# Optimization experiments

Measured on AMD Instinct MI355X. Metric: run time of the kernel, lower is better.

## Reference

```python
import jax, jax.numpy as jnp
import numpy as np

B, S, DIM = 2, 512, 4096
SMAX = 4096
HQ, HKV, HD = 32, 8, 128
REP = HQ // HKV
THETA = 1e6
NEG = -1e9  # stands in for -inf in the causal mask (safe under softmax/vjp)


def setup_inputs() -> dict:
    key = jax.random.key(0)
    ks = jax.random.split(key, 8)
    x = jax.random.normal(ks[0], (B, S, DIM), jnp.float32)
    # RoPE tables (complex freqs_cis represented as cos/sin), rope_theta=1e6
    inv = 1.0 / (THETA ** (np.arange(0, HD, 2, dtype=np.float64) / HD))
    ang = np.arange(SMAX, dtype=np.float64)[:, None] * inv[None, :]
    freqs_cos = jnp.asarray(np.cos(ang), jnp.float32)  # [SMAX, HD//2]
    freqs_sin = jnp.asarray(np.sin(ang), jnp.float32)
    cache = jax.random.normal(ks[1], (2, 1, B, SMAX, HKV, HD), jnp.float32) * 0.02
    i = np.arange(SMAX)
    mask = jnp.asarray(np.where(i[None, :] <= i[:, None], 0.0, NEG), jnp.float32)
    storage_idx = jnp.arange(S, dtype=jnp.int32)
    sc = 0.02
    wq = jax.random.normal(ks[2], (HQ * HD, DIM), jnp.float32) * sc
    wk = jax.random.normal(ks[3], (HKV * HD, DIM), jnp.float32) * sc
    wv = jax.random.normal(ks[4], (HKV * HD, DIM), jnp.float32) * sc
    wo = jax.random.normal(ks[5], (DIM, HQ * HD), jnp.float32) * sc
    return {"x": x, "freqs_cos": freqs_cos, "freqs_sin": freqs_sin, "cache": cache,
            "mask": mask, "storage_idx": storage_idx, "wq": wq, "wk": wk, "wv": wv, "wo": wo}


def _rope(t, c, s):
    # t: [B,S,H,HD]; consecutive pairs (2i, 2i+1) form complex numbers
    tr = t.reshape(*t.shape[:-1], -1, 2)
    a, b = tr[..., 0], tr[..., 1]
    o0 = a * c - b * s
    o1 = a * s + b * c
    return jnp.stack([o0, o1], axis=-1).reshape(t.shape)


def reference(x, freqs_cos, freqs_sin, cache, mask, storage_idx, wq, wk, wv, wo):
    bsz, seqlen, _ = x.shape
    hd = cache.shape[-1]
    hkv = cache.shape[-2]
    hq = wq.shape[0] // hd
    rep = hq // hkv
    xq = (x @ wq.T).reshape(bsz, seqlen, hq, hd)
    xk = (x @ wk.T).reshape(bsz, seqlen, hkv, hd)
    xv = (x @ wv.T).reshape(bsz, seqlen, hkv, hd)
    c = freqs_cos[storage_idx][None, :, None, :]  # [1,S,1,HD//2]
    s = freqs_sin[storage_idx][None, :, None, :]
    xq = _rope(xq, c, s)
    xk = _rope(xk, c, s)
    # rotating-cache write (index_copy along seq dim of cache[0/1, li])
    k_cache = cache[0, 0].at[:, storage_idx].set(xk)  # [B,SMAX,HKV,HD]
    v_cache = cache[1, 0].at[:, storage_idx].set(xv)
    keys = jnp.repeat(k_cache, rep, axis=2)    # GQA expand -> [B,SMAX,HQ,HD]
    values = jnp.repeat(v_cache, rep, axis=2)
    # NOTE: faithful to source: scores = QK^T / (head_dim ** -0.5)
    scores = jnp.einsum('bqhd,bkhd->bhqk', xq, keys) / (hd ** -0.5)
    scores = scores + mask[storage_idx][None, None, :, :]
    probs = jax.nn.softmax(scores.astype(jnp.float32), axis=-1).astype(xq.dtype)
    out = jnp.einsum('bhqk,bkhd->bqhd', probs, values).reshape(bsz, seqlen, hq * hd)
    return out @ wo.T
```

## Files before the change

kernel.cpp:

```cpp
#include <hip/hip_runtime.h>

#define Bn   2
#define Sn   512
#define DIMn 4096
#define HQn  32
#define HKVn 8
#define HDn  128
#define NPAIR 64
#define KVN  (HKVn * HDn)
#define NALL (DIMn + 2 * KVN)
#define SCALE 11.313708498984761f

typedef short bf16x8 __attribute__((ext_vector_type(8)));
typedef float f32x4 __attribute__((ext_vector_type(4)));
typedef unsigned short ushort8 __attribute__((ext_vector_type(8)));
typedef unsigned short ushort4s __attribute__((ext_vector_type(4)));
typedef int i32x4 __attribute__((ext_vector_type(4)));

__device__ __forceinline__ unsigned short f2bf_rne(float f) {
  unsigned u = __builtin_bit_cast(unsigned, f);
  u += 0x7fffu + ((u >> 16) & 1u);
  return (unsigned short)(u >> 16);
}
__device__ __forceinline__ float bf2f(unsigned short h) {
  unsigned u = ((unsigned)h) << 16;
  return __builtin_bit_cast(float, u);
}
__device__ __forceinline__ void split_bf16(float x, unsigned short& hi, unsigned short& lo) {
  unsigned u = __builtin_bit_cast(unsigned, x);
  hi = (unsigned short)(u >> 16);
  float hf = __builtin_bit_cast(float, u & 0xffff0000u);
  lo = (unsigned short)(__builtin_bit_cast(unsigned, x - hf) >> 16);
}
__device__ __forceinline__ void gload16(const void* g, void* lds) {
  __builtin_amdgcn_global_load_lds(
      (const __attribute__((address_space(1))) unsigned int*)g,
      (__attribute__((address_space(3))) unsigned int*)lds, 16, 0, 0);
}

__global__ __launch_bounds__(256) void quant_rows(
    const float* __restrict__ x, const float* __restrict__ wq,
    const float* __restrict__ wk, const float* __restrict__ wv,
    const float* __restrict__ wo,
    signed char* __restrict__ xh8, signed char* __restrict__ xl8,
    signed char* __restrict__ wh8, signed char* __restrict__ wl8,
    unsigned short* __restrict__ woh,
    float* __restrict__ sA, float* __restrict__ sW)
{
  const int r = blockIdx.x;
  const int t = threadIdx.x;

  if (r >= 1024 + NALL) {
    int wr2 = r - 1024 - NALL;
    const float* src = wo + (size_t)wr2 * DIMn;
    unsigned short* dst = woh + (size_t)wr2 * DIMn;
    #pragma unroll
    for (int j = 0; j < 4; ++j) {
      float4 v = ((const float4*)src)[t + j * 256];
      ushort4s h;
      h[0] = f2bf_rne(v.x); h[1] = f2bf_rne(v.y);
      h[2] = f2bf_rne(v.z); h[3] = f2bf_rne(v.w);
      ((ushort4s*)dst)[t + j * 256] = h;
    }
    return;
  }

  const float* src; signed char* ph; signed char* pl; float* ps; size_t prow;
  if (r < 1024) {
    src = x + (size_t)r * DIMn; ph = xh8; pl = xl8; ps = sA + r; prow = (size_t)r * DIMn;
  } else {
    int wr_ = r - 1024;
    ps = sW + wr_; ph = wh8; pl = wl8; prow = (size_t)wr_ * DIMn;
    if (wr_ < DIMn)            src = wq + (size_t)wr_ * DIMn;
    else if (wr_ < DIMn + KVN) src = wk + (size_t)(wr_ - DIMn) * DIMn;
    else                       src = wv + (size_t)(wr_ - DIMn - KVN) * DIMn;
  }
  float4 v[4];
  float am = 0.f;
  #pragma unroll
  for (int j = 0; j < 4; ++j) {
    v[j] = ((const float4*)src)[t + j * 256];
    am = fmaxf(am, fmaxf(fmaxf(fabsf(v[j].x), fabsf(v[j].y)),
                         fmaxf(fabsf(v[j].z), fabsf(v[j].w))));
  }
  #pragma unroll
  for (int o = 1; o < 64; o <<= 1) am = fmaxf(am, __shfl_xor(am, o));
  __shared__ float wm[4];
  if ((t & 63) == 0) wm[t >> 6] = am;
  __syncthreads();
  am = fmaxf(fmaxf(wm[0], wm[1]), fmaxf(wm[2], wm[3]));
  const float inv = (am > 0.f) ? 32512.0f / am : 0.f;
  if (t == 0) *ps = am * (1.0f / 32512.0f);
  #pragma unroll
  for (int j = 0; j < 4; ++j) {
    float fv[4] = {v[j].x, v[j].y, v[j].z, v[j].w};
    signed char hh[4], ll[4];
    #pragma unroll
    for (int e = 0; e < 4; ++e) {
      int q = __float2int_rn(fv[e] * inv);
      int hi = (q + 128) >> 8;
      hh[e] = (signed char)hi;
      ll[e] = (signed char)(q - (hi << 8));
    }
    ((char4*)(ph + prow))[t + j * 256] = make_char4(hh[0], hh[1], hh[2], hh[3]);
    ((char4*)(pl + prow))[t + j * 256] = make_char4(ll[0], ll[1], ll[2], ll[3]);
  }
}

__global__ __launch_bounds__(256, 2) void qkv_gemm_i8(
    const signed char* __restrict__ Ah, const signed char* __restrict__ Al,
    const signed char* __restrict__ Wh, const signed char* __restrict__ Wl,
    const float* __restrict__ sA, const float* __restrict__ sW,
    float* __restrict__ CQ, float* __restrict__ CK, unsigned short* __restrict__ CV)
{
  constexpr int KS = 64;
  constexpr int TILEB = 224 * 128;
  __shared__ __align__(16) signed char Ls[2][TILEB];

  const int t = threadIdx.x, w = t >> 6, lane = t & 63;
  const int bid = blockIdx.x;
  const int s = (bid & 7) * 64 + (bid >> 3);
  const int bx = s >> 3, by = s & 7;
  const int bm = by * 128, bn = bx * 96;

  const signed char* gsrc[7];
  int ldst[7];
  #pragma unroll
  for (int j = 0; j < 4; ++j) {
    int u = j * 256 + t;
    int R = u >> 3, slot = u & 7;
    int q = slot ^ (R & 7);
    gsrc[j] = (q < 4 ? Ah : Al) + (size_t)(bm + R) * DIMn + (q & 3) * 16;
    ldst[j] = u * 16;
  }
  #pragma unroll
  for (int j = 4; j < 7; ++j) {
    int base0 = (j - 4) * 16;
    int rb = base0 + (t >> 3) + ((t < 128) ? 0 : 32);
    int slot = t & 7;
    int q = slot ^ (rb & 7);
    gsrc[j] = (q < 4 ? Wh : Wl) + (size_t)(bn + rb) * DIMn + (q & 3) * 16;
    ldst[j] = (128 + rb) * 128 + slot * 16;
  }

  const int wr = w >> 1, wc = w & 1;
  const int rl = lane & 15, kh = lane >> 4;
  int aoff[4], boff[3];
  #pragma unroll
  for (int fm = 0; fm < 4; ++fm) {
    int R = wr * 64 + fm * 16 + rl;
    aoff[fm] = R * 128 + ((kh ^ (R & 7)) * 16);
  }
  #pragma unroll
  for (int fn = 0; fn < 3; ++fn) {
    int R = 128 + wc * 48 + fn * 16 + rl;
    boff[fn] = R * 128 + ((kh ^ (R & 7)) * 16);
  }

  i32x4 acc1[4][3], acc2[4][3];
  #pragma unroll
  for (int i = 0; i < 4; ++i)
  #pragma unroll
    for (int j = 0; j < 3; ++j) {
      acc1[i][j] = (i32x4){0, 0, 0, 0};
      acc2[i][j] = (i32x4){0, 0, 0, 0};
    }

  const int nt = DIMn / KS;
  #pragma unroll
  for (int j = 0; j < 7; ++j) gload16(gsrc[j], &Ls[0][ldst[j]]);

  for (int tt = 0; tt < nt; ++tt) {
    const int buf = tt & 1, nbuf = buf ^ 1;
    const bool more = (tt + 1 < nt);
    const signed char* Lp = &Ls[buf][0];
    i32x4 ah[4], al[4];

    asm volatile("s_waitcnt vmcnt(2)" ::: "memory");
    __builtin_amdgcn_s_barrier();
    __builtin_amdgcn_sched_barrier(0);
    if (more) {
      #pragma unroll
      for (int j = 0; j < 5; ++j)
        gload16(gsrc[j] + (size_t)(tt + 1) * KS, &Ls[nbuf][ldst[j]]);
    }
    #pragma unroll
    for (int fm = 0; fm < 4; ++fm) {
      ah[fm] = *(const i32x4*)(Lp + aoff[fm]);
      al[fm] = *(const i32x4*)(Lp + (aoff[fm] ^ 64));
    }
    {
      i32x4 bh = *(const i32x4*)(Lp + boff[0]);
      i32x4 bl = *(const i32x4*)(Lp + (boff[0] ^ 64));
      __builtin_amdgcn_s_setprio(1);
      #pragma unroll
      for (int fm = 0; fm < 4; ++fm) {
        acc1[fm][0] = __builtin_amdgcn_mfma_i32_16x16x64_i8(ah[fm], bh, acc1[fm][0], 0, 0, 0);
        acc2[fm][0] = __builtin_amdgcn_mfma_i32_16x16x64_i8(ah[fm], bl, acc2[fm][0], 0, 0, 0);
        acc2[fm][0] = __builtin_amdgcn_mfma_i32_16x16x64_i8(al[fm], bh, acc2[fm][0], 0, 0, 0);
      }
      __builtin_amdgcn_s_setprio(0);
    }

    if (more) asm volatile("s_waitcnt vmcnt(6)" ::: "memory");
    else      asm volatile("s_waitcnt vmcnt(1)" ::: "memory");
    __builtin_amdgcn_s_barrier();
    __builtin_amdgcn_sched_barrier(0);
    if (more)
      gload16(gsrc[5] + (size_t)(tt + 1) * KS, &Ls[nbuf][ldst[5]]);
    {
      i32x4 bh = *(const i32x4*)(Lp + boff[1]);
      i32x4 bl = *(const i32x4*)(Lp + (boff[1] ^ 64));
      __builtin_amdgcn_s_setprio(1);
      #pragma unroll
      for (int fm = 0; fm < 4; ++fm) {
        acc1[fm][1] = __builtin_amdgcn_mfma_i32_16x16x64_i8(ah[fm], bh, acc1[fm][1], 0, 0, 0);
        acc2[fm][1] = __builtin_amdgcn_mfma_i32_16x16x64_i8(ah[fm], bl, acc2[fm][1], 0, 0, 0);
        acc2[fm][1] = __builtin_amdgcn_mfma_i32_16x16x64_i8(al[fm], bh, acc2[fm][1], 0, 0, 0);
      }
      __builtin_amdgcn_s_setprio(0);
    }

    if (more) asm volatile("s_waitcnt vmcnt(6)" ::: "memory");
    else      asm volatile("s_waitcnt vmcnt(0)" ::: "memory");
    __builtin_amdgcn_s_barrier();
    __builtin_amdgcn_sched_barrier(0);
    if (more)
      gload16(gsrc[6] + (size_t)(tt + 1) * KS, &Ls[nbuf][ldst[6]]);
    {
      i32x4 bh = *(const i32x4*)(Lp + boff[2]);
      i32x4 bl = *(const i32x4*)(Lp + (boff[2] ^ 64));
      __builtin_amdgcn_s_setprio(1);
      #pragma unroll
      for (int fm = 0; fm < 4; ++fm) {
        acc1[fm][2] = __builtin_amdgcn_mfma_i32_16x16x64_i8(ah[fm], bh, acc1[fm][2], 0, 0, 0);
        acc2[fm][2] = __builtin_amdgcn_mfma_i32_16x16x64_i8(ah[fm], bl, acc2[fm][2], 0, 0, 0);
        acc2[fm][2] = __builtin_amdgcn_mfma_i32_16x16x64_i8(al[fm], bh, acc2[fm][2], 0, 0, 0);
      }
      __builtin_amdgcn_s_setprio(0);
    }
  }

  #pragma unroll
  for (int fn = 0; fn < 3; ++fn) {
    const int colW = bn + wc * 48 + fn * 16 + rl;
    const float sw = sW[colW];
    #pragma unroll
    for (int fm = 0; fm < 4; ++fm) {
      #pragma unroll
      for (int j = 0; j < 4; ++j) {
        int grow = bm + wr * 64 + fm * 16 + kh * 4 + j;
        float val = sA[grow] * sw *
            fmaf((float)acc1[fm][fn][j], 65536.0f, (float)acc2[fm][fn][j] * 256.0f);
        if (colW < DIMn)            CQ[(size_t)grow * DIMn + colW] = val;
        else if (colW < DIMn + KVN) CK[(size_t)grow * KVN + (colW - DIMn)] = val;
        else                        CV[(size_t)grow * KVN + (colW - DIMn - KVN)] = f2bf_rne(val);
      }
    }
  }
}

template<bool SPLIT, int OMODE>
__global__ __launch_bounds__(256, 2) void pgemm3(
    const unsigned short* __restrict__ Ah, const unsigned short* __restrict__ Al,
    const unsigned short* __restrict__ Wh, const unsigned short* __restrict__ Wl,
    void* __restrict__ C0, void* __restrict__ C1, void* __restrict__ C2, int Kd)
{
  constexpr int BM = 128, BN = 64;
  constexpr int ROWS = BM + BN;
  constexpr int UPT = ROWS / 32;
  constexpr int KS = SPLIT ? 32 : 64;
  constexpr int TILEB = ROWS * 128;

  __shared__ __align__(16) unsigned char Ls[3 * TILEB];

  const int t = threadIdx.x, w = t >> 6, lane = t & 63;
  const int bid = blockIdx.x;
  const int s = (bid & 7) * 64 + (bid >> 3);
  const int bm = (s & 7) * BM, bn = (s >> 3) * BN;

  const unsigned short* gsrc[UPT];
  #pragma unroll
  for (int j = 0; j < UPT; ++j) {
    int u = j * 256 + t;
    int R = u >> 3;
    int q = (u & 7) ^ (R & 7);
    int chunk = SPLIT ? (q & 3) : q;
    bool lo_ = SPLIT && (q >= 4);
    const unsigned short* base = (R < BM) ? (lo_ ? Al : Ah) : (lo_ ? Wl : Wh);
    int rg = (R < BM) ? (bm + R) : (bn + (R - BM));
    gsrc[j] = base + (size_t)rg * Kd + chunk * 8;
  }

  const int wr = w >> 1, wc = w & 1;
  const int rl = lane & 15, kh = lane >> 4;
  int aoff[4], boff[2];
  #pragma unroll
  for (int fm = 0; fm < 4; ++fm) {
    int r = wr * 64 + fm * 16 + rl;
    aoff[fm] = r * 128 + ((kh ^ (r & 7)) * 16);
  }
  #pragma unroll
  for (int fn = 0; fn < 2; ++fn) {
    int r = BM + wc * 32 + fn * 16 + rl;
    boff[fn] = r * 128 + ((kh ^ (r & 7)) * 16);
  }

  f32x4 acc[4][2];
  #pragma unroll
  for (int i = 0; i < 4; ++i)
  #pragma unroll
    for (int j = 0; j < 2; ++j) acc[i][j] = (f32x4){0.f, 0.f, 0.f, 0.f};

  const int nt = Kd / KS;
  #pragma unroll
  for (int j = 0; j < UPT; ++j) gload16(gsrc[j], &Ls[0 * TILEB + (j * 256 + t) * 16]);
  #pragma unroll
  for (int j = 0; j < UPT; ++j) gload16(gsrc[j] + KS, &Ls[1 * TILEB + (j * 256 + t) * 16]);

  int cur = 0;
  for (int tt = 0; tt < nt; ++tt) {
    if (tt + 1 < nt) asm volatile("s_waitcnt vmcnt(%0)" :: "n"(UPT) : "memory");
    else             asm volatile("s_waitcnt vmcnt(0)" ::: "memory");
    __builtin_amdgcn_s_barrier();
    __builtin_amdgcn_sched_barrier(0);

    int pre = cur + 2; if (pre >= 3) pre -= 3;
    if (tt + 2 < nt) {
      #pragma unroll
      for (int j = 0; j < UPT; ++j)
        gload16(gsrc[j] + (size_t)(tt + 2) * KS, &Ls[pre * TILEB + (j * 256 + t) * 16]);
    }

    const unsigned char* Lp = &Ls[cur * TILEB];
    bf16x8 a0[4], a1[4], b0[2], b1[2];
    #pragma unroll
    for (int fm = 0; fm < 4; ++fm) {
      a0[fm] = *(const bf16x8*)(Lp + aoff[fm]);
      a1[fm] = *(const bf16x8*)(Lp + (aoff[fm] ^ 64));
    }
    #pragma unroll
    for (int fn = 0; fn < 2; ++fn) {
      b0[fn] = *(const bf16x8*)(Lp + boff[fn]);
      b1[fn] = *(const bf16x8*)(Lp + (boff[fn] ^ 64));
    }
    __builtin_amdgcn_s_setprio(1);
    #pragma unroll
    for (int fm = 0; fm < 4; ++fm)
    #pragma unroll
      for (int fn = 0; fn < 2; ++fn) {
        if constexpr (SPLIT) {
          acc[fm][fn] = __builtin_amdgcn_mfma_f32_16x16x32_bf16(a0[fm], b0[fn], acc[fm][fn], 0, 0, 0);
          acc[fm][fn] = __builtin_amdgcn_mfma_f32_16x16x32_bf16(a1[fm], b0[fn], acc[fm][fn], 0, 0, 0);
          acc[fm][fn] = __builtin_amdgcn_mfma_f32_16x16x32_bf16(a0[fm], b1[fn], acc[fm][fn], 0, 0, 0);
        } else {
          acc[fm][fn] = __builtin_amdgcn_mfma_f32_16x16x32_bf16(a0[fm], b0[fn], acc[fm][fn], 0, 0, 0);
          acc[fm][fn] = __builtin_amdgcn_mfma_f32_16x16x32_bf16(a1[fm], b1[fn], acc[fm][fn], 0, 0, 0);
        }
      }
    __builtin_amdgcn_s_setprio(0);
    cur += 1; if (cur >= 3) cur -= 3;
  }

  const int crow0 = bm + wr * 64 + kh * 4;
  #pragma unroll
  for (int fm = 0; fm < 4; ++fm)
  #pragma unroll
    for (int fn = 0; fn < 2; ++fn)
    #pragma unroll
      for (int j = 0; j < 4; ++j) {
        int row = crow0 + fm * 16 + j;
        float v = acc[fm][fn][j];
        int col = bn + wc * 32 + fn * 16 + rl;
        if constexpr (OMODE == 0) {
          ((float*)C0)[(size_t)row * DIMn + col] = v;
        } else {
          if (col < DIMn)
            ((float*)C0)[(size_t)row * DIMn + col] = v;
          else if (col < DIMn + KVN)
            ((float*)C1)[(size_t)row * KVN + (col - DIMn)] = v;
          else
            ((unsigned short*)C2)[(size_t)row * KVN + (col - DIMn - KVN)] = f2bf_rne(v);
        }
      }
}

template<bool SPLIT, int BN>
__global__ __launch_bounds__(256, 2) void gemm_mfma(
    const float* __restrict__ A,
    const float* __restrict__ W0, float* __restrict__ C0,
    const float* __restrict__ W1, float* __restrict__ C1,
    int Kd, int N)
{
  constexpr int BM = 64;
  constexpr int KSTEP = SPLIT ? 32 : 64;
  constexpr int CPR = SPLIT ? 4 : 8;
  constexpr int AUNITS = BM * KSTEP / 8;
  constexpr int UNITS  = (BM + BN) * KSTEP / 8;
  constexpr int UPT = UNITS / 256;
  constexpr int FN = BN / 32;
  constexpr int ROWS = BM + BN;

  __shared__ __align__(16) unsigned short Ls[2][ROWS * 64];

  const float* __restrict__ W = (blockIdx.z == 0) ? W0 : W1;
  float* __restrict__ Cp = (blockIdx.z == 0) ? C0 : C1;

  const int t  = threadIdx.x;
  const int bm = blockIdx.y * BM;
  const int bn = blockIdx.x * BN;

  const float* gsrc[UPT];
  int loff[UPT];
  #pragma unroll
  for (int i = 0; i < UPT; ++i) {
    int u = i * 256 + t;
    int row, c;
    if (u < AUNITS) {
      row = u / CPR; c = u % CPR;
      gsrc[i] = A + (size_t)(bm + row) * Kd + c * 8;
    } else {
      int v = u - AUNITS;
      int rr = v / CPR; c = v % CPR;
      row = BM + rr;
      gsrc[i] = W + (size_t)(bn + rr) * Kd + c * 8;
    }
    loff[i] = row * 64 + (c ^ (row & 7)) * 8;
  }

  const int lane = t & 63;
  const int w  = t >> 6;
  const int wr = w >> 1, wc = w & 1;
  const int rl = lane & 15, kh = lane >> 4;

  int aoff[2], boff[FN];
  #pragma unroll
  for (int fm = 0; fm < 2; ++fm) {
    int row = wr * 32 + fm * 16 + rl;
    aoff[fm] = row * 64 + (kh ^ (row & 7)) * 8;
  }
  #pragma unroll
  for (int fn = 0; fn < FN; ++fn) {
    int row = BM + wc * (BN / 2) + fn * 16 + rl;
    boff[fn] = row * 64 + (kh ^ (row & 7)) * 8;
  }

  f32x4 acc[2][FN];
  #pragma unroll
  for (int i = 0; i < 2; ++i)
  #pragma unroll
    for (int j = 0; j < FN; ++j) acc[i][j] = (f32x4){0.f, 0.f, 0.f, 0.f};

  float4 f0[UPT], f1[UPT];
  #pragma unroll
  for (int i = 0; i < UPT; ++i) {
    f0[i] = *(const float4*)(gsrc[i]);
    f1[i] = *(const float4*)(gsrc[i] + 4);
  }

  const int nt = Kd / KSTEP;
  for (int tt = 0; tt < nt; ++tt) {
    unsigned short* Lp = &Ls[tt & 1][0];
    #pragma unroll
    for (int i = 0; i < UPT; ++i) {
      float xv[8] = {f0[i].x, f0[i].y, f0[i].z, f0[i].w,
                     f1[i].x, f1[i].y, f1[i].z, f1[i].w};
      ushort8 hi, lo;
      #pragma unroll
      for (int j = 0; j < 8; ++j) {
        if constexpr (SPLIT) {
          unsigned short h_, l_;
          split_bf16(xv[j], h_, l_);
          hi[j] = h_; lo[j] = l_;
        } else {
          hi[j] = f2bf_rne(xv[j]);
          lo[j] = 0;
        }
      }
      *(ushort8*)(Lp + loff[i]) = hi;
      if constexpr (SPLIT)
        *(ushort8*)(((uintptr_t)(Lp + loff[i])) ^ 64) = lo;
    }
    if (tt + 1 < nt) {
      #pragma unroll
      for (int i = 0; i < UPT; ++i) {
        f0[i] = *(const float4*)(gsrc[i] + (size_t)(tt + 1) * KSTEP);
        f1[i] = *(const float4*)(gsrc[i] + (size_t)(tt + 1) * KSTEP + 4);
      }
    }
    __syncthreads();

    bf16x8 a0[2], a1[2], b0[FN], b1[FN];
    #pragma unroll
    for (int fm = 0; fm < 2; ++fm) {
      const unsigned short* p = Lp + aoff[fm];
      a0[fm] = *(const bf16x8*)p;
      a1[fm] = *(const bf16x8*)(((uintptr_t)p) ^ 64);
    }
    #pragma unroll
    for (int fn = 0; fn < FN; ++fn) {
      const unsigned short* p = Lp + boff[fn];
      b0[fn] = *(const bf16x8*)p;
      b1[fn] = *(const bf16x8*)(((uintptr_t)p) ^ 64);
    }
    #pragma unroll
    for (int fm = 0; fm < 2; ++fm)
    #pragma unroll
      for (int fn = 0; fn < FN; ++fn) {
        if constexpr (SPLIT) {
          acc[fm][fn] = __builtin_amdgcn_mfma_f32_16x16x32_bf16(a0[fm], b0[fn], acc[fm][fn], 0, 0, 0);
          acc[fm][fn] = __builtin_amdgcn_mfma_f32_16x16x32_bf16(a1[fm], b0[fn], acc[fm][fn], 0, 0, 0);
          acc[fm][fn] = __builtin_amdgcn_mfma_f32_16x16x32_bf16(a0[fm], b1[fn], acc[fm][fn], 0, 0, 0);
        } else {
          acc[fm][fn] = __builtin_amdgcn_mfma_f32_16x16x32_bf16(a0[fm], b0[fn], acc[fm][fn], 0, 0, 0);
          acc[fm][fn] = __builtin_amdgcn_mfma_f32_16x16x32_bf16(a1[fm], b1[fn], acc[fm][fn], 0, 0, 0);
        }
      }
  }

  const int crow0 = bm + wr * 32 + kh * 4;
  const int ccol0 = bn + wc * (BN / 2) + rl;
  #pragma unroll
  for (int fm = 0; fm < 2; ++fm)
  #pragma unroll
    for (int fn = 0; fn < FN; ++fn)
    #pragma unroll
      for (int j = 0; j < 4; ++j)
        Cp[(size_t)(crow0 + fm * 16 + j) * N + ccol0 + fn * 16] = acc[fm][fn][j];
}

#define KT 32

template<bool BF16IO>
__global__ __launch_bounds__(256, 2) void flash_attn_mfma(
    const float* __restrict__ Qg, const float* __restrict__ Kg, const void* __restrict__ Vgv,
    const float* __restrict__ fc, const float* __restrict__ fs,
    const int* __restrict__ sidx, void* __restrict__ Ov)
{
  const int bid = blockIdx.x;
  const int qt = bid & 7;
  const int h  = (bid >> 3) & 31;
  const int b  = bid >> 8;
  const int q0 = qt * 64;
  const int hk = h >> 2;

  __shared__ __align__(16) unsigned short Ks[2][2][32][128];
  __shared__ __align__(16) unsigned short Vt[2][128][40];

  const int t = threadIdx.x;
  const int w = t >> 6;
  const int lane = t & 63;
  const int rl = lane & 15;
  const int kh = lane >> 4;

  const int qrow = q0 + w * 16 + rl;
  const int qp = sidx[qrow];

  int kr[2], kc_[2];
  #pragma unroll
  for (int i = 0; i < 2; ++i) { int u = i * 256 + t; kr[i] = u >> 4; kc_[i] = u & 15; }
  const int kkv = t >> 3, dcv = t & 7;

  const int nkt = (q0 + 64) / KT;
  const int qmaxw = q0 + w * 16 + 15;

  float kreg[2][8]; float4 kc4[2], ks4[2];
  float vregf[16];
  ushort8 vregu[2];

  #pragma unroll
  for (int i = 0; i < 2; ++i) {
    const float* kp_ = Kg + ((size_t)(b * Sn + kr[i]) * HKVn + hk) * HDn + kc_[i] * 8;
    *(float4*)&kreg[i][0] = *(const float4*)kp_;
    *(float4*)&kreg[i][4] = *(const float4*)(kp_ + 4);
    int posk = sidx[kr[i]];
    kc4[i] = *(const float4*)(fc + (size_t)posk * NPAIR + kc_[i] * 4);
    ks4[i] = *(const float4*)(fs + (size_t)posk * NPAIR + kc_[i] * 4);
  }
  if constexpr (BF16IO) {
    const unsigned short* vp_ = (const unsigned short*)Vgv +
        ((size_t)(b * Sn + kkv) * HKVn + hk) * HDn + dcv * 16;
    vregu[0] = *(const ushort8*)vp_;
    vregu[1] = *(const ushort8*)(vp_ + 8);
  } else {
    const float* vp_ = (const float*)Vgv + ((size_t)(b * Sn + kkv) * HKVn + hk) * HDn + dcv * 16;
    #pragma unroll
    for (int i = 0; i < 4; ++i) *(float4*)&vregf[i * 4] = *(const float4*)(vp_ + i * 4);
  }

  bf16x8 qh[4], ql[4];
  {
    const float* qptr = Qg + ((size_t)(b * Sn + qrow) * HQn + h) * HDn;
    #pragma unroll
    for (int ds = 0; ds < 4; ++ds) {
      int d0 = ds * 32 + kh * 8;
      float4 u0 = *(const float4*)(qptr + d0);
      float4 u1 = *(const float4*)(qptr + d0 + 4);
      float4 c4 = *(const float4*)(fc + (size_t)qp * NPAIR + d0 / 2);
      float4 s4 = *(const float4*)(fs + (size_t)qp * NPAIR + d0 / 2);
      float v[8];
      v[0] = u0.x * c4.x - u0.y * s4.x;  v[1] = u0.x * s4.x + u0.y * c4.x;
      v[2] = u0.z * c4.y - u0.w * s4.y;  v[3] = u0.z * s4.y + u0.w * c4.y;
      v[4] = u1.x * c4.z - u1.y * s4.z;  v[5] = u1.x * s4.z + u1.y * c4.z;
      v[6] = u1.z * c4.w - u1.w * s4.w;  v[7] = u1.z * s4.w + u1.w * c4.w;
      #pragma unroll
      for (int j = 0; j < 8; ++j) {
        unsigned short h_, l_;
        split_bf16(v[j], h_, l_);
        qh[ds][j] = (short)h_; ql[ds][j] = (short)l_;
      }
    }
  }

  float m_run = -3.0e38f, l_run = 0.f;
  f32x4 acc_o[8];
  #pragma unroll
  for (int i = 0; i < 8; ++i) acc_o[i] = (f32x4){0.f, 0.f, 0.f, 0.f};

  for (int tt = 0; tt < nkt; ++tt) {
    const int kbase = tt * KT;
    const int buf = tt & 1;

    #pragma unroll
    for (int i = 0; i < 2; ++i) {
      float rv[8];
      rv[0] = kreg[i][0] * kc4[i].x - kreg[i][1] * ks4[i].x;
      rv[1] = kreg[i][0] * ks4[i].x + kreg[i][1] * kc4[i].x;
      rv[2] = kreg[i][2] * kc4[i].y - kreg[i][3] * ks4[i].y;
      rv[3] = kreg[i][2] * ks4[i].y + kreg[i][3] * kc4[i].y;
      rv[4] = kreg[i][4] * kc4[i].z - kreg[i][5] * ks4[i].z;
      rv[5] = kreg[i][4] * ks4[i].z + kreg[i][5] * kc4[i].z;
      rv[6] = kreg[i][6] * kc4[i].w - kreg[i][7] * ks4[i].w;
      rv[7] = kreg[i][6] * ks4[i].w + kreg[i][7] * kc4[i].w;
      ushort8 hi, lo;
      #pragma unroll
      for (int j = 0; j < 8; ++j) {
        unsigned short h_, l_;
        split_bf16(rv[j], h_, l_);
        hi[j] = h_; lo[j] = l_;
      }
      int slot = kc_[i] ^ (kr[i] & 15);
      *(ushort8*)&Ks[buf][0][kr[i]][slot * 8] = hi;
      *(ushort8*)&Ks[buf][1][kr[i]][slot * 8] = lo;
    }
    if constexpr (BF16IO) {
      #pragma unroll
      for (int i = 0; i < 8; ++i) {
        Vt[buf][dcv * 16 + i][kkv] = vregu[0][i];
        Vt[buf][dcv * 16 + 8 + i][kkv] = vregu[1][i];
      }
    } else {
      #pragma unroll
      for (int i = 0; i < 16; ++i)
        Vt[buf][dcv * 16 + i][kkv] = f2bf_rne(vregf[i]);
    }

    if (tt + 1 < nkt) {
      const int kb = kbase + KT;
      #pragma unroll
      for (int i = 0; i < 2; ++i) {
        const float* kp_ = Kg + ((size_t)(b * Sn + kb + kr[i]) * HKVn + hk) * HDn + kc_[i] * 8;
        *(float4*)&kreg[i][0] = *(const float4*)kp_;
        *(float4*)&kreg[i][4] = *(const float4*)(kp_ + 4);
        int posk = sidx[kb + kr[i]];
        kc4[i] = *(const float4*)(fc + (size_t)posk * NPAIR + kc_[i] * 4);
        ks4[i] = *(const float4*)(fs + (size_t)posk * NPAIR + kc_[i] * 4);
      }
      if constexpr (BF16IO) {
        const unsigned short* vp_ = (const unsigned short*)Vgv +
            ((size_t)(b * Sn + kb + kkv) * HKVn + hk) * HDn + dcv * 16;
        vregu[0] = *(const ushort8*)vp_;
        vregu[1] = *(const ushort8*)(vp_ + 8);
      } else {
        const float* vp_ = (const float*)Vgv + ((size_t)(b * Sn + kb + kkv) * HKVn + hk) * HDn + dcv * 16;
        #pragma unroll
        for (int i = 0; i < 4; ++i) *(float4*)&vregf[i * 4] = *(const float4*)(vp_ + i * 4);
      }
    }
    __syncthreads();

    if (kbase > qmaxw) continue;

    float p[8];
    #pragma unroll
    for (int fm = 0; fm < 2; ++fm) {
      f32x4 accs = (f32x4){0.f, 0.f, 0.f, 0.f};
      #pragma unroll
      for (int ds = 0; ds < 4; ++ds) {
        int slot = (ds * 4 + kh) ^ rl;
        bf16x8 kH = *(const bf16x8*)&Ks[buf][0][fm * 16 + rl][slot * 8];
        bf16x8 kL = *(const bf16x8*)&Ks[buf][1][fm * 16 + rl][slot * 8];
        accs = __builtin_amdgcn_mfma_f32_16x16x32_bf16(kH, qh[ds], accs, 0, 0, 0);
        accs = __builtin_amdgcn_mfma_f32_16x16x32_bf16(kL, qh[ds], accs, 0, 0, 0);
        accs = __builtin_amdgcn_mfma_f32_16x16x32_bf16(kH, ql[ds], accs, 0, 0, 0);
      }
      #pragma unroll
      for (int r = 0; r < 4; ++r) {
        int kp = kbase + fm * 16 + kh * 4 + r;
        p[fm * 4 + r] = accs[r] * SCALE + ((kp <= qp) ? 0.f : -1.0e9f);
      }
    }

    float tmax = p[0];
    #pragma unroll
    for (int i = 1; i < 8; ++i) tmax = fmaxf(tmax, p[i]);
    tmax = fmaxf(tmax, __shfl_xor(tmax, 16));
    tmax = fmaxf(tmax, __shfl_xor(tmax, 32));
    float m_new = fmaxf(m_run, tmax);
    float crs = __expf(m_run - m_new);
    m_run = m_new;
    float tsum = 0.f;
    bf16x8 pa;
    #pragma unroll
    for (int i = 0; i < 8; ++i) {
      float ev = __expf(p[i] - m_new);
      tsum += ev;
      pa[i] = (short)f2bf_rne(ev);
    }
    tsum += __shfl_xor(tsum, 16);
    tsum += __shfl_xor(tsum, 32);
    l_run = l_run * crs + tsum;

    float cq[4];
    #pragma unroll
    for (int r = 0; r < 4; ++r) cq[r] = __shfl(crs, kh * 4 + r);

    #pragma unroll
    for (int db = 0; db < 8; ++db) {
      short4 v0 = *(const short4*)&Vt[buf][db * 16 + rl][kh * 4];
      short4 v1 = *(const short4*)&Vt[buf][db * 16 + rl][16 + kh * 4];
      bf16x8 vb = {v0.x, v0.y, v0.z, v0.w, v1.x, v1.y, v1.z, v1.w};
      f32x4 a = acc_o[db];
      a[0] *= cq[0]; a[1] *= cq[1]; a[2] *= cq[2]; a[3] *= cq[3];
      acc_o[db] = __builtin_amdgcn_mfma_f32_16x16x32_bf16(pa, vb, a, 0, 0, 0);
    }
  }

  float lq[4];
  #pragma unroll
  for (int r = 0; r < 4; ++r) lq[r] = 1.0f / __shfl(l_run, kh * 4 + r);
  #pragma unroll
  for (int db = 0; db < 8; ++db)
  #pragma unroll
    for (int r = 0; r < 4; ++r) {
      int q = q0 + w * 16 + kh * 4 + r;
      size_t idx = ((size_t)(b * Sn + q) * HQn + h) * HDn + db * 16 + rl;
      float val = acc_o[db][r] * lq[r];
      if constexpr (BF16IO) ((unsigned short*)Ov)[idx] = f2bf_rne(val);
      else                  ((float*)Ov)[idx] = val;
    }
}

extern "C" void kernel_launch(void* const* d_in, const int* in_sizes, int n_in,
                              void* d_out, int out_size, void* d_ws, size_t ws_size,
                              hipStream_t stream)
{
  const float* x    = (const float*)d_in[0];
  const float* fc   = (const float*)d_in[1];
  const float* fs   = (const float*)d_in[2];
  const int*   sidx = (const int*)d_in[5];
  const float* wq   = (const float*)d_in[6];
  const float* wk   = (const float*)d_in[7];
  const float* wv   = (const float*)d_in[8];
  const float* wo   = (const float*)d_in[9];
  float* out = (float*)d_out;

  const int M = Bn * Sn;
  const size_t EX  = (size_t)M * DIMn;
  const size_t EW  = (size_t)DIMn * DIMn;
  const size_t EK  = (size_t)M * KVN;
  const size_t EX8 = EX;
  const size_t EW8 = (size_t)NALL * DIMn;

  char* p = (char*)d_ws;
  signed char* xh8 = (signed char*)p;        p += EX8;
  signed char* xl8 = (signed char*)p;        p += EX8;
  signed char* wh8 = (signed char*)p;        p += EW8;
  signed char* wl8 = (signed char*)p;        p += EW8;
  float* sA = (float*)p;                     p += 1024 * 4;
  float* sW = (float*)p;                     p += (size_t)NALL * 4;
  float* Qw = (float*)p;                     p += 4 * EX;
  float* Kw = (float*)p;                     p += 4 * EK;
  unsigned short* Vw = (unsigned short*)p;   p += 2 * EK;
  unsigned short* woh = (unsigned short*)p;  p += 2 * EW;
  unsigned short* Aw = (unsigned short*)p;   p += 2 * EX;
  const size_t NEED = (size_t)(p - (char*)d_ws);

  if (ws_size >= NEED) {
    quant_rows<<<1024 + NALL + DIMn, 256, 0, stream>>>(
        x, wq, wk, wv, wo, xh8, xl8, wh8, wl8, woh, sA, sW);
    qkv_gemm_i8<<<512, 256, 0, stream>>>(
        xh8, xl8, wh8, wl8, sA, sW, Qw, Kw, Vw);
    flash_attn_mfma<true><<<Bn * HQn * (Sn / 64), 256, 0, stream>>>(
        Qw, Kw, Vw, fc, fs, sidx, Aw);
    pgemm3<false, 0><<<512, 256, 0, stream>>>(
        Aw, Aw, woh, woh, out, nullptr, nullptr, DIMn);
  } else {
    float* Qw2 = (float*)d_ws;
    float* Kw2 = Qw2 + (size_t)M * HQn * HDn;
    float* Vw2 = Kw2 + (size_t)M * HKVn * HDn;
    float* Aw2 = Vw2 + (size_t)M * HKVn * HDn;
    gemm_mfma<true, 128><<<dim3(DIMn / 128, M / 64, 1), 256, 0, stream>>>(
        x, wq, Qw2, wq, Qw2, DIMn, DIMn);
    gemm_mfma<true, 64><<<dim3((HKVn * HDn) / 64, M / 64, 2), 256, 0, stream>>>(
        x, wk, Kw2, wv, Vw2, DIMn, HKVn * HDn);
    flash_attn_mfma<false><<<Bn * HQn * (Sn / 64), 256, 0, stream>>>(
        Qw2, Kw2, Vw2, fc, fs, sidx, Aw2);
    gemm_mfma<false, 128><<<dim3(DIMn / 128, M / 64, 1), 256, 0, stream>>>(
        Aw2, wo, out, wo, out, DIMn, DIMn);
  }
}
```

Before: 215.9 us.

## Quantize output projection to int8 with per-row weight and global activation scales

Replaces the bf16 output-projection GEMM with an int8 MFMA GEMM. Wo is quantized per row to int8 inside the prep kernel. The attention kernel now tracks a global abs-max of its output through an atomic, and a new kernel quantizes the bf16 attention output to int8 with that single scale. This halves operand bytes and uses the faster int8 MFMA rate, at the cost of an extra quantization pass, an atomic reduction, and coarser numerical precision from per-tensor activation scaling.

```diff
diff --git a/kernel.cpp b/kernel.cpp
--- a/kernel.cpp
+++ b/kernel.cpp
@@ -14,7 +14,7 @@
 typedef short bf16x8 __attribute__((ext_vector_type(8)));
 typedef float f32x4 __attribute__((ext_vector_type(4)));
 typedef unsigned short ushort8 __attribute__((ext_vector_type(8)));
-typedef unsigned short ushort4s __attribute__((ext_vector_type(4)));
+typedef signed char char8 __attribute__((ext_vector_type(8)));
 typedef int i32x4 __attribute__((ext_vector_type(4)));
 
 __device__ __forceinline__ unsigned short f2bf_rne(float f) {
@@ -44,23 +44,44 @@
     const float* __restrict__ wo,
     signed char* __restrict__ xh8, signed char* __restrict__ xl8,
     signed char* __restrict__ wh8, signed char* __restrict__ wl8,
-    unsigned short* __restrict__ woh,
-    float* __restrict__ sA, float* __restrict__ sW)
+    signed char* __restrict__ wo8,
+    float* __restrict__ sA, float* __restrict__ sW, float* __restrict__ sWo,
+    unsigned* __restrict__ amaxp)
 {
   const int r = blockIdx.x;
   const int t = threadIdx.x;
+  if (r == 0 && t == 0) *amaxp = 0u;
+
+  __shared__ float wm[4];
 
   if (r >= 1024 + NALL) {
     int wr2 = r - 1024 - NALL;
     const float* src = wo + (size_t)wr2 * DIMn;
-    unsigned short* dst = woh + (size_t)wr2 * DIMn;
+    float4 v[4];
+    float am = 0.f;
     #pragma unroll
     for (int j = 0; j < 4; ++j) {
-      float4 v = ((const float4*)src)[t + j * 256];
-      ushort4s h;
-      h[0] = f2bf_rne(v.x); h[1] = f2bf_rne(v.y);
-      h[2] = f2bf_rne(v.z); h[3] = f2bf_rne(v.w);
-      ((ushort4s*)dst)[t + j * 256] = h;
+      v[j] = ((const float4*)src)[t + j * 256];
+      am = fmaxf(am, fmaxf(fmaxf(fabsf(v[j].x), fabsf(v[j].y)),
+                           fmaxf(fabsf(v[j].z), fabsf(v[j].w))));
+    }
+    #pragma unroll
+    for (int o = 1; o < 64; o <<= 1) am = fmaxf(am, __shfl_xor(am, o));
+    if ((t & 63) == 0) wm[t >> 6] = am;
+    __syncthreads();
+    am = fmaxf(fmaxf(wm[0], wm[1]), fmaxf(wm[2], wm[3]));
+    const float inv = (am > 0.f) ? 127.0f / am : 0.f;
+    if (t == 0) sWo[wr2] = am * (1.0f / 127.0f);
+    signed char* dst = wo8 + (size_t)wr2 * DIMn;
+    #pragma unroll
+    for (int j = 0; j < 4; ++j) {
+      float fv[4] = {v[j].x, v[j].y, v[j].z, v[j].w};
+      char4 q;
+      q.x = (signed char)__float2int_rn(fv[0] * inv);
+      q.y = (signed char)__float2int_rn(fv[1] * inv);
+      q.z = (signed char)__float2int_rn(fv[2] * inv);
+      q.w = (signed char)__float2int_rn(fv[3] * inv);
+      ((char4*)dst)[t + j * 256] = q;
     }
     return;
   }
@@ -85,7 +106,6 @@
   }
   #pragma unroll
   for (int o = 1; o < 64; o <<= 1) am = fmaxf(am, __shfl_xor(am, o));
-  __shared__ float wm[4];
   if ((t & 63) == 0) wm[t >> 6] = am;
   __syncthreads();
   am = fmaxf(fmaxf(wm[0], wm[1]), fmaxf(wm[2], wm[3]));
@@ -105,6 +125,22 @@
     ((char4*)(ph + prow))[t + j * 256] = make_char4(hh[0], hh[1], hh[2], hh[3]);
     ((char4*)(pl + prow))[t + j * 256] = make_char4(ll[0], ll[1], ll[2], ll[3]);
   }
+}
+
+__global__ __launch_bounds__(256) void aquant_k(
+    const unsigned short* __restrict__ Aw, signed char* __restrict__ A8,
+    const unsigned* __restrict__ amaxp, int n8)
+{
+  const float am = __builtin_bit_cast(float, *amaxp);
+  const float inv = (am > 0.f) ? 127.0f / am : 0.f;
+  int i = blockIdx.x * blockDim.x + threadIdx.x;
+  if (i >= n8) return;
+  ushort8 a = ((const ushort8*)Aw)[i];
+  char8 q;
+  #pragma unroll
+  for (int j = 0; j < 8; ++j)
+    q[j] = (signed char)__float2int_rn(bf2f(a[j]) * inv);
+  ((char8*)A8)[i] = q;
 }
 
 __global__ __launch_bounds__(256, 2) void qkv_gemm_i8(
@@ -260,36 +296,29 @@
   }
 }
 
-template<bool SPLIT, int OMODE>
-__global__ __launch_bounds__(256, 2) void pgemm3(
-    const unsigned short* __restrict__ Ah, const unsigned short* __restrict__ Al,
-    const unsigned short* __restrict__ Wh, const unsigned short* __restrict__ Wl,
-    void* __restrict__ C0, void* __restrict__ C1, void* __restrict__ C2, int Kd)
+__global__ __launch_bounds__(256, 2) void oproj_i8(
+    const signed char* __restrict__ A8, const signed char* __restrict__ Wo8,
+    const float* __restrict__ sWo, const unsigned* __restrict__ amaxp,
+    float* __restrict__ out)
 {
-  constexpr int BM = 128, BN = 64;
-  constexpr int ROWS = BM + BN;
-  constexpr int UPT = ROWS / 32;
-  constexpr int KS = SPLIT ? 32 : 64;
-  constexpr int TILEB = ROWS * 128;
-
-  __shared__ __align__(16) unsigned char Ls[3 * TILEB];
+  constexpr int KS = 128;
+  constexpr int TILEB = 192 * 128;
+  __shared__ __align__(16) signed char Ls[3 * TILEB];
 
   const int t = threadIdx.x, w = t >> 6, lane = t & 63;
   const int bid = blockIdx.x;
   const int s = (bid & 7) * 64 + (bid >> 3);
-  const int bm = (s & 7) * BM, bn = (s >> 3) * BN;
-
-  const unsigned short* gsrc[UPT];
-  #pragma unroll
-  for (int j = 0; j < UPT; ++j) {
+  const int bm = (s & 7) * 128, bn = (s >> 3) * 64;
+
+  const signed char* gsrc[6];
+  #pragma unroll
+  for (int j = 0; j < 6; ++j) {
     int u = j * 256 + t;
-    int R = u >> 3;
-    int q = (u & 7) ^ (R & 7);
-    int chunk = SPLIT ? (q & 3) : q;
-    bool lo_ = SPLIT && (q >= 4);
-    const unsigned short* base = (R < BM) ? (lo_ ? Al : Ah) : (lo_ ? Wl : Wh);
-    int rg = (R < BM) ? (bm + R) : (bn + (R - BM));
-    gsrc[j] = base + (size_t)rg * Kd + chunk * 8;
+    int R = u >> 3, slot = u & 7;
+    int q = slot ^ (R & 7);
+    const signed char* base = (R < 128) ? A8 : Wo8;
+    int rg = (R < 128) ? (bm + R) : (bn + (R - 128));
+    gsrc[j] = base + (size_t)rg * DIMn + q * 16;
   }
 
   const int wr = w >> 1, wc = w & 1;
@@ -297,30 +326,30 @@
   int aoff[4], boff[2];
   #pragma unroll
   for (int fm = 0; fm < 4; ++fm) {
-    int r = wr * 64 + fm * 16 + rl;
-    aoff[fm] = r * 128 + ((kh ^ (r & 7)) * 16);
+    int R = wr * 64 + fm * 16 + rl;
+    aoff[fm] = R * 128 + ((kh ^ (R & 7)) * 16);
   }
   #pragma unroll
   for (int fn = 0; fn < 2; ++fn) {
-    int r = BM + wc * 32 + fn * 16 + rl;
-    boff[fn] = r * 128 + ((kh ^ (r & 7)) * 16);
-  }
-
-  f32x4 acc[4][2];
+    int R = 128 + wc * 32 + fn * 16 + rl;
+    boff[fn] = R * 128 + ((kh ^ (R & 7)) * 16);
+  }
+
+  i32x4 acc[4][2];
   #pragma unroll
   for (int i = 0; i < 4; ++i)
   #pragma unroll
-    for (int j = 0; j < 2; ++j) acc[i][j] = (f32x4){0.f, 0.f, 0.f, 0.f};
-
-  const int nt = Kd / KS;
-  #pragma unroll
-  for (int j = 0; j < UPT; ++j) gload16(gsrc[j], &Ls[0 * TILEB + (j * 256 + t) * 16]);
-  #pragma unroll
-  for (int j = 0; j < UPT; ++j) gload16(gsrc[j] + KS, &Ls[1 * TILEB + (j * 256 + t) * 16]);
+    for (int j = 0; j < 2; ++j) acc[i][j] = (i32x4){0, 0, 0, 0};
+
+  const int nt = DIMn / KS;
+  #pragma unroll
+  for (int j = 0; j < 6; ++j) gload16(gsrc[j], &Ls[0 * TILEB + (j * 256 + t) * 16]);
+  #pragma unroll
+  for (int j = 0; j < 6; ++j) gload16(gsrc[j] + KS, &Ls[1 * TILEB + (j * 256 + t) * 16]);
 
   int cur = 0;
   for (int tt = 0; tt < nt; ++tt) {
-    if (tt + 1 < nt) asm volatile("s_waitcnt vmcnt(%0)" :: "n"(UPT) : "memory");
+    if (tt + 1 < nt) asm volatile("s_waitcnt vmcnt(6)" ::: "memory");
     else             asm volatile("s_waitcnt vmcnt(0)" ::: "memory");
     __builtin_amdgcn_s_barrier();
     __builtin_amdgcn_sched_barrier(0);
@@ -328,61 +357,46 @@
     int pre = cur + 2; if (pre >= 3) pre -= 3;
     if (tt + 2 < nt) {
       #pragma unroll
-      for (int j = 0; j < UPT; ++j)
+      for (int j = 0; j < 6; ++j)
         gload16(gsrc[j] + (size_t)(tt + 2) * KS, &Ls[pre * TILEB + (j * 256 + t) * 16]);
     }
 
-    const unsigned char* Lp = &Ls[cur * TILEB];
-    bf16x8 a0[4], a1[4], b0[2], b1[2];
+    const signed char* Lp = &Ls[cur * TILEB];
+    i32x4 a0[4], a1[4], b0[2], b1[2];
     #pragma unroll
     for (int fm = 0; fm < 4; ++fm) {
-      a0[fm] = *(const bf16x8*)(Lp + aoff[fm]);
-      a1[fm] = *(const bf16x8*)(Lp + (aoff[fm] ^ 64));
+      a0[fm] = *(const i32x4*)(Lp + aoff[fm]);
+      a1[fm] = *(const i32x4*)(Lp + (aoff[fm] ^ 64));
     }
     #pragma unroll
     for (int fn = 0; fn < 2; ++fn) {
-      b0[fn] = *(const bf16x8*)(Lp + boff[fn]);
-      b1[fn] = *(const bf16x8*)(Lp + (boff[fn] ^ 64));
+      b0[fn] = *(const i32x4*)(Lp + boff[fn]);
+      b1[fn] = *(const i32x4*)(Lp + (boff[fn] ^ 64));
     }
     __builtin_amdgcn_s_setprio(1);
     #pragma unroll
     for (int fm = 0; fm < 4; ++fm)
     #pragma unroll
       for (int fn = 0; fn < 2; ++fn) {
-        if constexpr (SPLIT) {
-          acc[fm][fn] = __builtin_amdgcn_mfma_f32_16x16x32_bf16(a0[fm], b0[fn], acc[fm][fn], 0, 0, 0);
-          acc[fm][fn] = __builtin_amdgcn_mfma_f32_16x16x32_bf16(a1[fm], b0[fn], acc[fm][fn], 0, 0, 0);
-          acc[fm][fn] = __builtin_amdgcn_mfma_f32_16x16x32_bf16(a0[fm], b1[fn], acc[fm][fn], 0, 0, 0);
-        } else {
-          acc[fm][fn] = __builtin_amdgcn_mfma_f32_16x16x32_bf16(a0[fm], b0[fn], acc[fm][fn], 0, 0, 0);
-          acc[fm][fn] = __builtin_amdgcn_mfma_f32_16x16x32_bf16(a1[fm], b1[fn], acc[fm][fn], 0, 0, 0);
-        }
+        acc[fm][fn] = __builtin_amdgcn_mfma_i32_16x16x64_i8(a0[fm], b0[fn], acc[fm][fn], 0, 0, 0);
+        acc[fm][fn] = __builtin_amdgcn_mfma_i32_16x16x64_i8(a1[fm], b1[fn], acc[fm][fn], 0, 0, 0);
       }
     __builtin_amdgcn_s_setprio(0);
     cur += 1; if (cur >= 3) cur -= 3;
   }
 
+  const float sAg = __builtin_bit_cast(float, *amaxp) * (1.0f / 127.0f);
   const int crow0 = bm + wr * 64 + kh * 4;
   #pragma unroll
-  for (int fm = 0; fm < 4; ++fm)
-  #pragma unroll
-    for (int fn = 0; fn < 2; ++fn)
-    #pragma unroll
-      for (int j = 0; j < 4; ++j) {
-        int row = crow0 + fm * 16 + j;
-        float v = acc[fm][fn][j];
-        int col = bn + wc * 32 + fn * 16 + rl;
-        if constexpr (OMODE == 0) {
-          ((float*)C0)[(size_t)row * DIMn + col] = v;
-        } else {
-          if (col < DIMn)
-            ((float*)C0)[(size_t)row * DIMn + col] = v;
-          else if (col < DIMn + KVN)
-            ((float*)C1)[(size_t)row * KVN + (col - DIMn)] = v;
-          else
-            ((unsigned short*)C2)[(size_t)row * KVN + (col - DIMn - KVN)] = f2bf_rne(v);
-        }
-      }
+  for (int fn = 0; fn < 2; ++fn) {
+    const int col = bn + wc * 32 + fn * 16 + rl;
+    const float sw = sWo[col] * sAg;
+    #pragma unroll
+    for (int fm = 0; fm < 4; ++fm)
+    #pragma unroll
+      for (int j = 0; j < 4; ++j)
+        out[(size_t)(crow0 + fm * 16 + j) * DIMn + col] = sw * (float)acc[fm][fn][j];
+  }
 }
 
 template<bool SPLIT, int BN>
@@ -531,11 +545,11 @@
 
 #define KT 32
 
-template<bool BF16IO>
+template<bool BF16IO, bool AMAX>
 __global__ __launch_bounds__(256, 2) void flash_attn_mfma(
     const float* __restrict__ Qg, const float* __restrict__ Kg, const void* __restrict__ Vgv,
     const float* __restrict__ fc, const float* __restrict__ fs,
-    const int* __restrict__ sidx, void* __restrict__ Ov)
+    const int* __restrict__ sidx, void* __restrict__ Ov, unsigned* __restrict__ amaxp)
 {
   const int bid = blockIdx.x;
   const int qt = bid & 7;
@@ -546,6 +560,7 @@
 
   __shared__ __align__(16) unsigned short Ks[2][2][32][128];
   __shared__ __align__(16) unsigned short Vt[2][128][40];
+  __shared__ float wmx[4];
 
   const int t = threadIdx.x;
   const int w = t >> 6;
@@ -739,6 +754,7 @@
   float lq[4];
   #pragma unroll
   for (int r = 0; r < 4; ++r) lq[r] = 1.0f / __shfl(l_run, kh * 4 + r);
+  float lmax = 0.f;
   #pragma unroll
   for (int db = 0; db < 8; ++db)
   #pragma unroll
@@ -746,9 +762,20 @@
       int q = q0 + w * 16 + kh * 4 + r;
       size_t idx = ((size_t)(b * Sn + q) * HQn + h) * HDn + db * 16 + rl;
       float val = acc_o[db][r] * lq[r];
+      if constexpr (AMAX) lmax = fmaxf(lmax, fabsf(val));
       if constexpr (BF16IO) ((unsigned short*)Ov)[idx] = f2bf_rne(val);
       else                  ((float*)Ov)[idx] = val;
     }
+  if constexpr (AMAX) {
+    #pragma unroll
+    for (int o = 1; o < 64; o <<= 1) lmax = fmaxf(lmax, __shfl_xor(lmax, o));
+    if (lane == 0) wmx[w] = lmax;
+    __syncthreads();
+    if (t == 0) {
+      float m = fmaxf(fmaxf(wmx[0], wmx[1]), fmaxf(wmx[2], wmx[3]));
+      atomicMax(amaxp, __builtin_bit_cast(unsigned, m));
+    }
+  }
 }
 
 extern "C" void kernel_launch(void* const* d_in, const int* in_sizes, int n_in,
@@ -769,43 +796,46 @@
   const size_t EX  = (size_t)M * DIMn;
   const size_t EW  = (size_t)DIMn * DIMn;
   const size_t EK  = (size_t)M * KVN;
-  const size_t EX8 = EX;
   const size_t EW8 = (size_t)NALL * DIMn;
 
   char* p = (char*)d_ws;
-  signed char* xh8 = (signed char*)p;        p += EX8;
-  signed char* xl8 = (signed char*)p;        p += EX8;
+  signed char* xh8 = (signed char*)p;        p += EX;
+  signed char* xl8 = (signed char*)p;        p += EX;
   signed char* wh8 = (signed char*)p;        p += EW8;
   signed char* wl8 = (signed char*)p;        p += EW8;
-  float* sA = (float*)p;                     p += 1024 * 4;
-  float* sW = (float*)p;                     p += (size_t)NALL * 4;
+  signed char* wo8 = (signed char*)p;        p += EW;
+  signed char* A8  = (signed char*)p;        p += EX;
+  float* sA  = (float*)p;                    p += 1024 * 4;
+  float* sW  = (float*)p;                    p += (size_t)NALL * 4;
+  float* sWo = (float*)p;                    p += (size_t)DIMn * 4;
+  unsigned* amaxp = (unsigned*)p;            p += 256;
   float* Qw = (float*)p;                     p += 4 * EX;
   float* Kw = (float*)p;                     p += 4 * EK;
   unsigned short* Vw = (unsigned short*)p;   p += 2 * EK;
-  unsigned short* woh = (unsigned short*)p;  p += 2 * EW;
   unsigned short* Aw = (unsigned short*)p;   p += 2 * EX;
   const size_t NEED = (size_t)(p - (char*)d_ws);
 
   if (ws_size >= NEED) {
     quant_rows<<<1024 + NALL + DIMn, 256, 0, stream>>>(
-        x, wq, wk, wv, wo, xh8, xl8, wh8, wl8, woh, sA, sW);
+        x, wq, wk, wv, wo, xh8, xl8, wh8, wl8, wo8, sA, sW, sWo, amaxp);
     qkv_gemm_i8<<<512, 256, 0, stream>>>(
         xh8, xl8, wh8, wl8, sA, sW, Qw, Kw, Vw);
-    flash_attn_mfma<true><<<Bn * HQn * (Sn / 64), 256, 0, stream>>>(
-        Qw, Kw, Vw, fc, fs, sidx, Aw);
-    pgemm3<false, 0><<<512, 256, 0, stream>>>(
-        Aw, Aw, woh, woh, out, nullptr, nullptr, DIMn);
+    flash_attn_mfma<true, true><<<Bn * HQn * (Sn / 64), 256, 0, stream>>>(
+        Qw, Kw, Vw, fc, fs, sidx, Aw, amaxp);
+    aquant_k<<<(int)(EX / 8 / 256), 256, 0, stream>>>(Aw, A8, amaxp, (int)(EX / 8));
+    oproj_i8<<<512, 256, 0, stream>>>(A8, wo8, sWo, amaxp, out);
   } else {
     float* Qw2 = (float*)d_ws;
     float* Kw2 = Qw2 + (size_t)M * HQn * HDn;
     float* Vw2 = Kw2 + (size_t)M * HKVn * HDn;
     float* Aw2 = Vw2 + (size_t)M * HKVn * HDn;
+    unsigned* dummyA = (unsigned*)(Aw2 + (size_t)M * HQn * HDn);
     gemm_mfma<true, 128><<<dim3(DIMn / 128, M / 64, 1), 256, 0, stream>>>(
         x, wq, Qw2, wq, Qw2, DIMn, DIMn);
     gemm_mfma<true, 64><<<dim3((HKVn * HDn) / 64, M / 64, 2), 256, 0, stream>>>(
         x, wk, Kw2, wv, Vw2, DIMn, HKVn * HDn);
-    flash_attn_mfma<false><<<Bn * HQn * (Sn / 64), 256, 0, stream>>>(
-        Qw2, Kw2, Vw2, fc, fs, sidx, Aw2);
+    flash_attn_mfma<false, false><<<Bn * HQn * (Sn / 64), 256, 0, stream>>>(
+        Qw2, Kw2, Vw2, fc, fs, sidx, Aw2, dummyA);
     gemm_mfma<false, 128><<<dim3(DIMn / 128, M / 64, 1), 256, 0, stream>>>(
         Aw2, wo, out, wo, out, DIMn, DIMn);
   }
```

Result: faster. 199.9 us (-7.4%).
